# Performance work log

Measured on AMD Instinct MI355X. Metric: run time of the kernel, lower is better.

The kernel has to match this reference:

```python
import jax, jax.numpy as jnp
import numpy as np

E, H, F = 1024, 16, 4096
WH, WW = 32, 32
B = 4
L = WH * WW           # 1024 cross-attn kv tokens
N = L + 1             # 1025 decoder tokens (CLS + window)
D = E // H
SCALE = D ** -0.5
NEG = -1e9            # stands in for -inf in the causal mask


def _rel_coords(Wh, Ww):
    coords = np.stack(np.meshgrid(np.arange(Wh), np.arange(Ww), indexing='ij')).reshape(2, -1)
    rc = (coords[:, :, None] - coords[:, None, :]).transpose(1, 2, 0).astype(np.int64)
    rc[:, :, 0] += Wh - 1
    rc[:, :, 1] += Ww - 1
    rc[:, :, 0] *= 2 * Ww - 1
    return rc.sum(-1)  # (L, L)


def rel_index_self(Wh, Ww):
    nrd = (2 * Wh - 1) * (2 * Ww - 1) + 3
    l = Wh * Ww
    idx = np.zeros((l + 1, l + 1), dtype=np.int32)
    idx[1:, 1:] = _rel_coords(Wh, Ww)
    idx[0, :] = nrd - 3
    idx[:, 0] = nrd - 2
    idx[0, 0] = nrd - 1
    return idx


def rel_index_cross(Wh, Ww):
    nrd = (2 * Wh - 1) * (2 * Ww - 1) + 1
    l = Wh * Ww
    idx = np.zeros((l + 1, l), dtype=np.int32)
    idx[1:, :] = _rel_coords(Wh, Ww)
    idx[0, :] = nrd - 1
    return idx


IDX_SELF = jnp.asarray(rel_index_self(WH, WW))    # (N, N) int32
IDX_CROSS = jnp.asarray(rel_index_cross(WH, WW))  # (N, L) int32
CAUSAL = jnp.triu(jnp.full((N, N), NEG, jnp.float32), 1)


def _ln(x, g, b, eps=1e-5):
    m = x.mean(-1, keepdims=True)
    v = ((x - m) ** 2).mean(-1, keepdims=True)
    return (x - m) * jax.lax.rsqrt(v + eps) * g + b


def setup_inputs():
    key = jax.random.key(0)
    ks = jax.random.split(key, 24)
    g = lambda i, shape, s=0.02: jax.random.normal(ks[i], shape, jnp.float32) * s
    return dict(
        x=g(0, (B, N, E), 1.0),
        y=g(1, (B, L, E), 1.0),
        norm1_g=jnp.ones((E,), jnp.float32), norm1_b=jnp.zeros((E,), jnp.float32),
        norm2_g=jnp.ones((E,), jnp.float32), norm2_b=jnp.zeros((E,), jnp.float32),
        norm3_g=jnp.ones((E,), jnp.float32), norm3_b=jnp.zeros((E,), jnp.float32),
        sa_qkv_w=g(2, (3 * E, E)),
        sa_q_bias=g(3, (E,)),
        sa_v_bias=g(4, (E,)),
        sa_rpb=g(5, ((2 * WH - 1) * (2 * WW - 1) + 3, H)),
        sa_proj_w=g(6, (E, E)), sa_proj_b=g(7, (E,)),
        ca_q_w=g(8, (E, E)),
        ca_kv_w=g(9, (2 * E, E)),
        ca_q_bias=g(10, (E,)),
        ca_v_bias=g(11, (E,)),
        ca_rpb=g(12, ((2 * WH - 1) * (2 * WW - 1) + 1, H)),
        ca_proj_w=g(13, (E, E)), ca_proj_b=g(14, (E,)),
        fc1_w=g(15, (F, E)), fc1_b=g(16, (F,)),
        fc2_w=g(17, (E, F)), fc2_b=g(18, (E,)),
        gamma1=jnp.full((E,), 0.1, jnp.float32),
        gamma2=jnp.full((E,), 0.1, jnp.float32),
        gamma3=jnp.full((E,), 0.1, jnp.float32),
    )


def reference(x, y, norm1_g, norm1_b, norm2_g, norm2_b, norm3_g, norm3_b,
              sa_qkv_w, sa_q_bias, sa_v_bias, sa_rpb, sa_proj_w, sa_proj_b,
              ca_q_w, ca_kv_w, ca_q_bias, ca_v_bias, ca_rpb, ca_proj_w, ca_proj_b,
              fc1_w, fc1_b, fc2_w, fc2_b, gamma1, gamma2, gamma3):
    # cross_attn.extract_kv(y): k gets zero bias, v gets v_bias
    kv_bias = jnp.concatenate([jnp.zeros((E,), x.dtype), ca_v_bias])
    kv = (y @ ca_kv_w.T + kv_bias).reshape(B, L, 2, H, D)
    ck = kv[:, :, 0].transpose(0, 2, 1, 3)  # (B,H,L,D)
    cv = kv[:, :, 1].transpose(0, 2, 1, 3)

    # --- causal self-attention with gathered relative-position bias ---
    h = _ln(x, norm1_g, norm1_b)
    qkv_bias = jnp.concatenate([sa_q_bias, jnp.zeros((E,), x.dtype), sa_v_bias])
    qkv = (h @ sa_qkv_w.T + qkv_bias).reshape(B, N, 3, H, D)
    q = qkv[:, :, 0].transpose(0, 2, 1, 3) * SCALE  # (B,H,N,D)
    k = qkv[:, :, 1].transpose(0, 2, 1, 3)
    v = qkv[:, :, 2].transpose(0, 2, 1, 3)
    bias = sa_rpb[IDX_SELF].transpose(2, 0, 1) + CAUSAL  # (H,N,N)
    attn = jnp.einsum('bhqd,bhkd->bhqk', q, k) + bias[None]
    attn = jax.nn.softmax(attn, axis=-1)
    sa = jnp.einsum('bhqk,bhkd->bhqd', attn, v).transpose(0, 2, 1, 3).reshape(B, N, E)
    sa = sa @ sa_proj_w.T + sa_proj_b
    x = x + gamma1 * sa

    # --- cross-attention with gathered relative-position bias ---
    h = _ln(x, norm2_g, norm2_b)
    q = (h @ ca_q_w.T + ca_q_bias).reshape(B, N, H, D).transpose(0, 2, 1, 3) * SCALE
    cbias = ca_rpb[IDX_CROSS].transpose(2, 0, 1)  # (H,N,L)
    attn = jnp.einsum('bhqd,bhkd->bhqk', q, ck) + cbias[None]
    attn = jax.nn.softmax(attn, axis=-1)
    ca = jnp.einsum('bhqk,bhkd->bhqd', attn, cv).transpose(0, 2, 1, 3).reshape(B, N, E)
    ca = ca @ ca_proj_w.T + ca_proj_b
    x = x + gamma2 * ca

    # --- FFN (Linear -> GELU -> Linear, no inner identity) ---
    h = _ln(x, norm3_g, norm3_b)
    h = jax.nn.gelu(h @ fc1_w.T + fc1_b, approximate=False)
    h = h @ fc2_w.T + fc2_b
    x = x + gamma3 * h
    return x
```

## Files before the change

kernel.cpp:

```cpp
#include <hip/hip_runtime.h>
#include <hip/hip_bf16.h>
#include <math.h>

typedef __bf16 bf16;
typedef __bf16 bf16x8 __attribute__((ext_vector_type(8)));
typedef float f32x4 __attribute__((ext_vector_type(4)));

#define MP    4224
#define MACT  4100
#define NQTOK 1025
#define NKTOK 1024
#define EDIM  1024
#define FDIM  4096
#define NHEAD 16
#define HD    64
#define QSCALE 0.125f
#define VTS   1056

__device__ __forceinline__ void glds16(const bf16* g, bf16* l) {
  __builtin_amdgcn_global_load_lds(
      (const __attribute__((address_space(1))) void*)g,
      (__attribute__((address_space(3))) void*)l, 16, 0, 0);
}

__device__ __forceinline__ bf16x8 ld8(const void* p, size_t i, bool f32) {
  if (f32) {
    const float* q = (const float*)p + i;
    bf16x8 r;
#pragma unroll
    for (int j = 0; j < 8; ++j) r[j] = (bf16)q[j];
    return r;
  }
  return *(const bf16x8*)((const bf16*)p + i);
}

struct WPtrs { const float* s[8]; };
__global__ __launch_bounds__(256) void conv_kernel(WPtrs wp, bf16* dst) {
  const size_t sz[8] = {3145728UL, 1048576UL, 1048576UL, 2097152UL,
                        1048576UL, 4194304UL, 4194304UL, 4194304UL};
  size_t id = ((size_t)blockIdx.x * 256 + threadIdx.x) * 8;
  size_t off = 0;
#pragma unroll
  for (int i = 0; i < 8; ++i) {
    if (id < off + sz[i]) {
      const float* s = wp.s[i] + (id - off);
      bf16x8 r;
#pragma unroll
      for (int j = 0; j < 8; ++j) r[j] = (bf16)s[j];
      *(bf16x8*)(dst + id) = r;
      return;
    }
    off += sz[i];
  }
}

__global__ void zero_pads_kernel(bf16* hln) {
  int i = blockIdx.x * 256 + threadIdx.x;
  const int n = (MP - MACT) * EDIM;
  if (i < n) hln[(size_t)MACT * EDIM + i] = (bf16)0.0f;
}

template<bool FIRST>
__global__ __launch_bounds__(256) void ln_kernel(const float* __restrict__ src,
    float* __restrict__ xf, bf16* __restrict__ out,
    const float* __restrict__ g, const float* __restrict__ bta) {
  const int row = blockIdx.x;
  const int tid = threadIdx.x;
  float v[4];
#pragma unroll
  for (int i = 0; i < 4; ++i) {
    v[i] = src[(size_t)row * EDIM + tid + i * 256];
    if (FIRST) xf[(size_t)row * EDIM + tid + i * 256] = v[i];
  }
  float s = 0.f, sq = 0.f;
#pragma unroll
  for (int i = 0; i < 4; ++i) { s += v[i]; sq += v[i] * v[i]; }
#pragma unroll
  for (int m = 32; m >= 1; m >>= 1) {
    s += __shfl_xor(s, m);
    sq += __shfl_xor(sq, m);
  }
  __shared__ float ss[4], ssq[4];
  const int wave = tid >> 6;
  if ((tid & 63) == 0) { ss[wave] = s; ssq[wave] = sq; }
  __syncthreads();
  s = ss[0] + ss[1] + ss[2] + ss[3];
  sq = ssq[0] + ssq[1] + ssq[2] + ssq[3];
  const float mean = s * (1.f / EDIM);
  const float var = sq * (1.f / EDIM) - mean * mean;
  const float rstd = rsqrtf(var + 1e-5f);
#pragma unroll
  for (int i = 0; i < 4; ++i) {
    int e = tid + i * 256;
    out[(size_t)row * EDIM + e] = (bf16)((v[i] - mean) * rstd * g[e] + bta[e]);
  }
}

__global__ __launch_bounds__(256) void fc2_reduce_kernel(
    const float* __restrict__ p0, const float* __restrict__ xf,
    const float* __restrict__ bias, const float* __restrict__ gamma,
    float* __restrict__ outf) {
  size_t i = ((size_t)blockIdx.x * 256 + threadIdx.x) * 4;
  if (i >= (size_t)MACT * EDIM) return;
  f32x4 a = *(const f32x4*)(p0 + i);
  f32x4 b = *(const f32x4*)(outf + i);
  f32x4 x = *(const f32x4*)(xf + i);
  const int gn = (int)(i & (EDIM - 1));
  f32x4 r;
#pragma unroll
  for (int j = 0; j < 4; ++j)
    r[j] = x[j] + gamma[gn + j] * (a[j] + b[j] + bias[gn + j]);
  *(f32x4*)(outf + i) = r;
}

enum { EPI_QKV = 0, EPI_KV = 1, EPI_Q = 2, EPI_RES = 3, EPI_GELU = 4,
       EPI_FINAL = 5, EPI_PART = 6 };

template<int EPI, bool ASY>
__global__ __launch_bounds__(256) void gemm_bt(
    const void* __restrict__ A, const void* __restrict__ Bw,
    int K, int Kc,
    const float* __restrict__ bias0, const float* __restrict__ bias1,
    const float* __restrict__ gamma, float* __restrict__ xf,
    bf16* __restrict__ out0, bf16* __restrict__ out1, bf16* __restrict__ out2,
    float* __restrict__ outf)
{
  constexpr int LDP = ASY ? 32 : 40;
  __shared__ bf16 As[128][LDP];
  __shared__ bf16 Bs[128][LDP];
  const int tid = threadIdx.x;
  const int lane = tid & 63, wave = tid >> 6;
  const int quad = lane >> 4, l16 = lane & 15;
  const int wr = wave >> 1, wc = wave & 1;
  const int m0 = blockIdx.y * 128, n0 = blockIdx.x * 128;
  const int kbase = blockIdx.z * Kc;
  const bool first = (blockIdx.z == 0);
  const int r0 = tid >> 2, c0 = (tid & 3) * 8;

  const bf16* gA = nullptr; const bf16* gB = nullptr;
  bf16* lA = nullptr; bf16* lB = nullptr;
  if (ASY) {
    gA = (const bf16*)A + (size_t)(m0 + wave * 16 + (lane >> 2)) * K + kbase + (lane & 3) * 8;
    gB = (const bf16*)Bw + (size_t)(n0 + wave * 16 + (lane >> 2)) * K + kbase + (lane & 3) * 8;
    lA = &As[wave * 16][0];
    lB = &Bs[wave * 16][0];
  }

  f32x4 acc[4][4];
#pragma unroll
  for (int i = 0; i < 4; ++i)
#pragma unroll
    for (int j = 0; j < 4; ++j)
#pragma unroll
      for (int r = 0; r < 4; ++r) acc[i][j][r] = 0.f;

  for (int k0 = 0; k0 < Kc; k0 += 32) {
    if (ASY) {
      glds16(gA, lA);
      glds16(gA + (size_t)64 * K, lA + 64 * 32);
      glds16(gB, lB);
      glds16(gB + (size_t)64 * K, lB + 64 * 32);
      gA += 32; gB += 32;
    } else {
      const bool f32a = (EPI == EPI_KV);
      const size_t kk = (size_t)(kbase + k0);
      *(bf16x8*)(&As[r0][c0])      = ld8(A,  (size_t)(m0 + r0) * K + kk + c0, f32a);
      *(bf16x8*)(&As[r0 + 64][c0]) = ld8(A,  (size_t)(m0 + r0 + 64) * K + kk + c0, f32a);
      *(bf16x8*)(&Bs[r0][c0])      = ld8(Bw, (size_t)(n0 + r0) * K + kk + c0, true);
      *(bf16x8*)(&Bs[r0 + 64][c0]) = ld8(Bw, (size_t)(n0 + r0 + 64) * K + kk + c0, true);
    }
    __syncthreads();
    bf16x8 af[4], bfv[4];
#pragma unroll
    for (int i = 0; i < 4; ++i) {
      af[i]  = *(const bf16x8*)(&As[wr * 64 + i * 16 + l16][quad * 8]);
      bfv[i] = *(const bf16x8*)(&Bs[wc * 64 + i * 16 + l16][quad * 8]);
    }
#pragma unroll
    for (int mb = 0; mb < 4; ++mb)
#pragma unroll
      for (int nb = 0; nb < 4; ++nb)
        acc[mb][nb] = __builtin_amdgcn_mfma_f32_16x16x32_bf16(af[mb], bfv[nb], acc[mb][nb], 0, 0, 0);
    __syncthreads();
  }

#pragma unroll
  for (int mb = 0; mb < 4; ++mb) {
#pragma unroll
    for (int r = 0; r < 4; ++r) {
      const int gm = m0 + wr * 64 + mb * 16 + quad * 4 + r;
#pragma unroll
      for (int nb = 0; nb < 4; ++nb) {
        const int gn = n0 + wc * 64 + nb * 16 + l16;
        float v = acc[mb][nb][r];
        if (EPI == EPI_QKV) {
          if (gm < MACT) {
            unsigned b = (unsigned)gm / 1025u;
            unsigned t = (unsigned)gm - b * 1025u;
            int sec = gn >> 10, e = gn & 1023;
            int h = e >> 6, d = e & 63;
            if (sec == 0)
              out0[((size_t)(b * NHEAD + h) * NQTOK + t) * HD + d] =
                  (bf16)((v + bias0[e]) * QSCALE);
            else if (sec == 1)
              out1[((size_t)(b * NHEAD + h) * NQTOK + t) * HD + d] = (bf16)v;
            else
              out2[((size_t)(b * NHEAD + h) * HD + d) * VTS + t] =
                  (bf16)(v + bias1[e]);
          }
        } else if (EPI == EPI_KV) {
          unsigned b = (unsigned)gm >> 10;
          unsigned t = (unsigned)gm & 1023u;
          int sec = gn >> 10, e = gn & 1023;
          int h = e >> 6, d = e & 63;
          if (sec == 0)
            out0[((size_t)(b * NHEAD + h) * NKTOK + t) * HD + d] = (bf16)v;
          else
            out1[((size_t)(b * NHEAD + h) * HD + d) * NKTOK + t] =
                (bf16)(v + bias1[e]);
        } else if (EPI == EPI_Q) {
          if (gm < MACT) {
            unsigned b = (unsigned)gm / 1025u;
            unsigned t = (unsigned)gm - b * 1025u;
            int h = gn >> 6, d = gn & 63;
            outf[((size_t)(b * NHEAD + h) * NQTOK + t) * HD + d] =
                (v + bias0[gn]) * QSCALE;
          }
        } else if (EPI == EPI_RES) {
          if (gm < MACT) {
            size_t o = (size_t)gm * EDIM + gn;
            xf[o] += gamma[gn] * (v + bias0[gn]);
          }
        } else if (EPI == EPI_GELU) {
          float z = v + bias0[gn];
          float ge = 0.5f * z * (1.0f + erff(z * 0.70710678118f));
          out0[(size_t)gm * FDIM + gn] = (bf16)ge;
        } else if (EPI == EPI_PART) {
          if (gm < MACT) {
            float* dst = first ? xf : outf;
            dst[(size_t)gm * EDIM + gn] = v;
          }
        } else {
          if (gm < MACT) {
            size_t o = (size_t)gm * EDIM + gn;
            float add = gamma[gn] * (v + (first ? bias0[gn] : 0.f));
            if (first) add += xf[o];
            atomicAdd(&outf[o], add);
          }
        }
      }
    }
  }
}

template<bool CROSS>
__global__ __launch_bounds__(256) void attn_kernel(
    const void* __restrict__ Q, const bf16* __restrict__ Kg,
    const bf16* __restrict__ Vg, const float* __restrict__ rpb,
    bf16* __restrict__ out)
{
  const int NK  = CROSS ? NKTOK : NQTOK;
  const int NRD = CROSS ? 3970 : 3972;
  const int VS  = CROSS ? NKTOK : VTS;
  const int qt  = CROSS ? blockIdx.x : (16 - blockIdx.x);
  const int h = blockIdx.y, b = blockIdx.z;
  const int tid = threadIdx.x;
  const int lane = tid & 63, wave = tid >> 6;
  const int quad = lane >> 4, l16 = lane & 15;

  __shared__ bf16 rpb_s[4096];
  __shared__ bf16 Ks[64][72];
  __shared__ bf16 Vt[64][72];
  __shared__ bf16 Ps[4][16][72];

  for (int i = tid; i < 4096; i += 256)
    rpb_s[i] = (bf16)((i < NRD) ? rpb[(size_t)i * NHEAD + h] : 0.f);

  const int q0 = qt * 64;
  const int qrow = q0 + wave * 16 + l16;
  const size_t qhb = (size_t)(b * NHEAD + h) * NQTOK;
  bf16x8 qf0, qf1;
  if (qrow < NQTOK) {
    if (CROSS) {
      const float* Qf = (const float*)Q + (qhb + qrow) * HD;
#pragma unroll
      for (int j = 0; j < 8; ++j) {
        qf0[j] = (bf16)Qf[quad * 8 + j];
        qf1[j] = (bf16)Qf[32 + quad * 8 + j];
      }
    } else {
      const bf16* Qb = (const bf16*)Q;
      qf0 = *(const bf16x8*)(Qb + (qhb + qrow) * HD + quad * 8);
      qf1 = *(const bf16x8*)(Qb + (qhb + qrow) * HD + 32 + quad * 8);
    }
  } else {
#pragma unroll
    for (int j = 0; j < 8; ++j) { qf0[j] = (bf16)0.f; qf1[j] = (bf16)0.f; }
  }

  int qgv[4], qcode[4];
#pragma unroll
  for (int r = 0; r < 4; ++r) {
    int qg = q0 + wave * 16 + quad * 4 + r;
    qgv[r] = qg;
    int p = qg - 1;
    qcode[r] = (qg > 0) ? ((p >> 5) * 63 + (p & 31) + 1984) : 0;
  }

  float m_run[4], l_run[4];
  f32x4 oacc[4];
#pragma unroll
  for (int r = 0; r < 4; ++r) { m_run[r] = -1e30f; l_run[r] = 0.f; }
#pragma unroll
  for (int d = 0; d < 4; ++d)
#pragma unroll
    for (int r = 0; r < 4; ++r) oacc[d][r] = 0.f;

  const size_t kvbK = (size_t)(b * NHEAD + h) * NK;
  const size_t vbase = (size_t)(b * NHEAD + h) * HD;
  const int nch = CROSS ? (NKTOK / 64) : (qt + 1);

  const int rr = tid >> 3;
  const int co = (tid & 7) * 8;

  bf16x8 krg[2], vrg[2];
  auto stage_load = [&](int c) {
    const int kc = c * 64;
#pragma unroll
    for (int vv = 0; vv < 2; ++vv) {
      const int row = rr + vv * 32;
      if (!CROSS && kc + row >= NK) {
#pragma unroll
        for (int j = 0; j < 8; ++j) krg[vv][j] = (bf16)0.f;
      } else {
        krg[vv] = *(const bf16x8*)(Kg + (kvbK + kc + row) * HD + co);
      }
      if (!CROSS && kc + co >= NK) {
#pragma unroll
        for (int j = 0; j < 8; ++j) vrg[vv][j] = (bf16)0.f;
      } else {
        vrg[vv] = *(const bf16x8*)(Vg + (vbase + row) * VS + kc + co);
      }
    }
  };

  stage_load(0);
  for (int c = 0; c < nch; ++c) {
    const int kc = c * 64;
    if (c) __syncthreads();
#pragma unroll
    for (int vv = 0; vv < 2; ++vv) {
      const int row = rr + vv * 32;
      *(bf16x8*)(&Ks[row][co]) = krg[vv];
      *(bf16x8*)(&Vt[row][co]) = vrg[vv];
    }
    __syncthreads();
    if (c + 1 < nch) stage_load(c + 1);

    float sv[4][4];
#pragma unroll
    for (int kb = 0; kb < 4; ++kb) {
      f32x4 a;
#pragma unroll
      for (int r = 0; r < 4; ++r) a[r] = 0.f;
      bf16x8 kf0 = *(const bf16x8*)(&Ks[kb * 16 + l16][quad * 8]);
      bf16x8 kf1 = *(const bf16x8*)(&Ks[kb * 16 + l16][32 + quad * 8]);
      a = __builtin_amdgcn_mfma_f32_16x16x32_bf16(qf0, kf0, a, 0, 0, 0);
      a = __builtin_amdgcn_mfma_f32_16x16x32_bf16(qf1, kf1, a, 0, 0, 0);
      const int kg = kc + kb * 16 + l16;
      int kcode;
      if (CROSS) kcode = (kg >> 5) * 63 + (kg & 31);
      else {
        int k1 = kg - 1;
        kcode = (kg > 0) ? ((k1 >> 5) * 63 + (k1 & 31)) : 0;
      }
#pragma unroll
      for (int r = 0; r < 4; ++r) {
        const int qg = qgv[r];
        bool valid = (kg < NK) && (CROSS || kg <= qg);
        int idx;
        if (CROSS) {
          idx = (qg == 0) ? 3969 : (qcode[r] - kcode);
        } else {
          idx = (qg == 0) ? ((kg == 0) ? 3971 : 3969)
                          : ((kg == 0) ? 3970 : (qcode[r] - kcode));
        }
        sv[kb][r] = valid ? (a[r] + (float)rpb_s[idx]) : -1e30f;
      }
    }

#pragma unroll
    for (int r = 0; r < 4; ++r) {
      float mx = fmaxf(fmaxf(sv[0][r], sv[1][r]), fmaxf(sv[2][r], sv[3][r]));
#pragma unroll
      for (int mk = 8; mk >= 1; mk >>= 1) mx = fmaxf(mx, __shfl_xor(mx, mk));
      const float mnew = fmaxf(m_run[r], mx);
      const float alpha = __expf(m_run[r] - mnew);
      m_run[r] = mnew;
      float rs = 0.f;
#pragma unroll
      for (int kb = 0; kb < 4; ++kb) {
        float p = __expf(sv[kb][r] - mnew);
        rs += p;
        Ps[wave][quad * 4 + r][kb * 16 + l16] = (bf16)p;
      }
#pragma unroll
      for (int mk = 8; mk >= 1; mk >>= 1) rs += __shfl_xor(rs, mk);
      l_run[r] = l_run[r] * alpha + rs;
#pragma unroll
      for (int d = 0; d < 4; ++d) oacc[d][r] *= alpha;
    }

    bf16x8 pf0 = *(const bf16x8*)(&Ps[wave][l16][quad * 8]);
    bf16x8 pf1 = *(const bf16x8*)(&Ps[wave][l16][32 + quad * 8]);
#pragma unroll
    for (int db = 0; db < 4; ++db) {
      bf16x8 vf0 = *(const bf16x8*)(&Vt[db * 16 + l16][quad * 8]);
      bf16x8 vf1 = *(const bf16x8*)(&Vt[db * 16 + l16][32 + quad * 8]);
      oacc[db] = __builtin_amdgcn_mfma_f32_16x16x32_bf16(pf0, vf0, oacc[db], 0, 0, 0);
      oacc[db] = __builtin_amdgcn_mfma_f32_16x16x32_bf16(pf1, vf1, oacc[db], 0, 0, 0);
    }
  }

#pragma unroll
  for (int r = 0; r < 4; ++r) {
    const int qg = qgv[r];
    if (qg < NQTOK) {
      const float inv = 1.f / l_run[r];
      const size_t row = (size_t)b * NQTOK + qg;
#pragma unroll
      for (int db = 0; db < 4; ++db)
        out[row * EDIM + h * HD + db * 16 + l16] = (bf16)(oacc[db][r] * inv);
    }
  }
}

extern "C" void kernel_launch(void* const* d_in, const int* in_sizes, int n_in,
                              void* d_out, int out_size, void* d_ws, size_t ws_size,
                              hipStream_t stream) {
  (void)in_sizes; (void)n_in; (void)out_size;
  const float* x        = (const float*)d_in[0];
  const float* y        = (const float*)d_in[1];
  const float* n1g      = (const float*)d_in[2];
  const float* n1b      = (const float*)d_in[3];
  const float* n2g      = (const float*)d_in[4];
  const float* n2b      = (const float*)d_in[5];
  const float* n3g      = (const float*)d_in[6];
  const float* n3b      = (const float*)d_in[7];
  const float* sa_qkv_w = (const float*)d_in[8];
  const float* sa_qb    = (const float*)d_in[9];
  const float* sa_vb    = (const float*)d_in[10];
  const float* sa_rpb   = (const float*)d_in[11];
  const float* sa_pw    = (const float*)d_in[12];
  const float* sa_pb    = (const float*)d_in[13];
  const float* ca_qw    = (const float*)d_in[14];
  const float* ca_kvw   = (const float*)d_in[15];
  const float* ca_qb    = (const float*)d_in[16];
  const float* ca_vb    = (const float*)d_in[17];
  const float* ca_rpb   = (const float*)d_in[18];
  const float* ca_pw    = (const float*)d_in[19];
  const float* ca_pb    = (const float*)d_in[20];
  const float* fc1_w    = (const float*)d_in[21];
  const float* fc1_b    = (const float*)d_in[22];
  const float* fc2_w    = (const float*)d_in[23];
  const float* fc2_b    = (const float*)d_in[24];
  const float* g1       = (const float*)d_in[25];
  const float* g2       = (const float*)d_in[26];
  const float* g3       = (const float*)d_in[27];
  float* outf = (float*)d_out;
  float* qtf  = (float*)d_out;

  char* w = (char*)d_ws;
  float* xf = (float*)w;  w += (size_t)MP * EDIM * 4;
  bf16* hln = (bf16*)w;   w += (size_t)MP * EDIM * 2;
  char* big = w;          w += (size_t)MP * FDIM * 2;
  const size_t qkv_sz = (size_t)4 * NHEAD * NQTOK * HD * 2;
  bf16* qt = (bf16*)big;
  bf16* kt = (bf16*)(big + qkv_sz);
  bf16* vt = (bf16*)(big + 2 * qkv_sz);
  bf16* h1 = (bf16*)big;
  bf16* wpool = (bf16*)w; w += 20971520UL * 2;
  const bool asy = ((size_t)(w - (char*)d_ws) <= ws_size);

  bf16* qkvw_b = wpool;
  bf16* pw_b   = qkvw_b + 3145728UL;
  bf16* cqw_b  = pw_b   + 1048576UL;
  bf16* ckvw_b = cqw_b  + 1048576UL;
  bf16* cpw_b  = ckvw_b + 2097152UL;
  bf16* fc1w_b = cpw_b  + 1048576UL;
  bf16* fc2w_b = fc1w_b + 4194304UL;
  bf16* y_b    = fc2w_b + 4194304UL;
  float* part0 = (float*)wpool;

  if (asy) {
    WPtrs wp = {{sa_qkv_w, sa_pw, ca_qw, ca_kvw, ca_pw, fc1_w, fc2_w, y}};
    conv_kernel<<<10240, 256, 0, stream>>>(wp, wpool);
  }
  zero_pads_kernel<<<dim3(((MP - MACT) * EDIM + 255) / 256), 256, 0, stream>>>(hln);

  ln_kernel<true><<<MACT, 256, 0, stream>>>(x, xf, hln, n1g, n1b);
  if (asy) gemm_bt<EPI_QKV, true><<<dim3(24, 33, 1), 256, 0, stream>>>(hln, qkvw_b, 1024, 1024,
      sa_qb, sa_vb, nullptr, nullptr, qt, kt, vt, nullptr);
  else     gemm_bt<EPI_QKV, false><<<dim3(24, 33, 1), 256, 0, stream>>>(hln, sa_qkv_w, 1024, 1024,
      sa_qb, sa_vb, nullptr, nullptr, qt, kt, vt, nullptr);
  attn_kernel<false><<<dim3(17, NHEAD, 4), 256, 0, stream>>>(qt, kt, vt, sa_rpb, hln);
  if (asy) gemm_bt<EPI_RES, true><<<dim3(8, 33, 1), 256, 0, stream>>>(hln, pw_b, 1024, 1024,
      sa_pb, nullptr, g1, xf, nullptr, nullptr, nullptr, nullptr);
  else     gemm_bt<EPI_RES, false><<<dim3(8, 33, 1), 256, 0, stream>>>(hln, sa_pw, 1024, 1024,
      sa_pb, nullptr, g1, xf, nullptr, nullptr, nullptr, nullptr);

  ln_kernel<false><<<MACT, 256, 0, stream>>>(xf, nullptr, hln, n2g, n2b);
  if (asy) gemm_bt<EPI_Q, true><<<dim3(8, 33, 1), 256, 0, stream>>>(hln, cqw_b, 1024, 1024,
      ca_qb, nullptr, nullptr, nullptr, nullptr, nullptr, nullptr, qtf);
  else     gemm_bt<EPI_Q, false><<<dim3(8, 33, 1), 256, 0, stream>>>(hln, ca_qw, 1024, 1024,
      ca_qb, nullptr, nullptr, nullptr, nullptr, nullptr, nullptr, qtf);
  if (asy) gemm_bt<EPI_KV, true><<<dim3(16, 32, 1), 256, 0, stream>>>(y_b, ckvw_b, 1024, 1024,
      nullptr, ca_vb, nullptr, nullptr, kt, vt, nullptr, nullptr);
  else     gemm_bt<EPI_KV, false><<<dim3(16, 32, 1), 256, 0, stream>>>(y, ca_kvw, 1024, 1024,
      nullptr, ca_vb, nullptr, nullptr, kt, vt, nullptr, nullptr);
  attn_kernel<true><<<dim3(17, NHEAD, 4), 256, 0, stream>>>(qtf, kt, vt, ca_rpb, hln);
  if (asy) gemm_bt<EPI_RES, true><<<dim3(8, 33, 1), 256, 0, stream>>>(hln, cpw_b, 1024, 1024,
      ca_pb, nullptr, g2, xf, nullptr, nullptr, nullptr, nullptr);
  else     gemm_bt<EPI_RES, false><<<dim3(8, 33, 1), 256, 0, stream>>>(hln, ca_pw, 1024, 1024,
      ca_pb, nullptr, g2, xf, nullptr, nullptr, nullptr, nullptr);

  ln_kernel<false><<<MACT, 256, 0, stream>>>(xf, nullptr, hln, n3g, n3b);
  if (asy) gemm_bt<EPI_GELU, true><<<dim3(32, 33, 1), 256, 0, stream>>>(hln, fc1w_b, 1024, 1024,
      fc1_b, nullptr, nullptr, nullptr, h1, nullptr, nullptr, nullptr);
  else     gemm_bt<EPI_GELU, false><<<dim3(32, 33, 1), 256, 0, stream>>>(hln, fc1_w, 1024, 1024,
      fc1_b, nullptr, nullptr, nullptr, h1, nullptr, nullptr, nullptr);
  if (asy) {
    gemm_bt<EPI_PART, true><<<dim3(8, 33, 2), 256, 0, stream>>>(h1, fc2w_b, 4096, 2048,
        nullptr, nullptr, nullptr, part0, nullptr, nullptr, nullptr, outf);
    fc2_reduce_kernel<<<dim3(4100), 256, 0, stream>>>(part0, xf, fc2_b, g3, outf);
  } else {
    hipMemsetAsync(outf, 0, (size_t)MACT * EDIM * 4, stream);
    gemm_bt<EPI_FINAL, false><<<dim3(8, 33, 4), 256, 0, stream>>>(h1, fc2_w, 4096, 1024,
        fc2_b, nullptr, g3, xf, nullptr, nullptr, nullptr, outf);
  }
}
```

Baseline: 746.7 us.

## Transpose QK MFMA to keep P in registers and defer softmax rescaling

The QK^T MFMA now swaps its operands, so each lane holds scores for a single query row across several keys. That makes the row max and sum need only two cross-quad shuffles instead of per-row 16-lane reductions. The probabilities are packed to bf16 and redistributed with lane shuffles into the PV A-operand layout, which removes the Ps shared-memory round trip. The running-max rescale of the accumulator is skipped unless the new max exceeds the old by more than 8, trading some headroom in the exponent range for fewer rescales.

```diff
diff --git a/kernel.cpp b/kernel.cpp
--- a/kernel.cpp
+++ b/kernel.cpp
@@ -271,7 +271,6 @@
   __shared__ bf16 rpb_s[4096];
   __shared__ bf16 Ks[64][72];
   __shared__ bf16 Vt[64][72];
-  __shared__ bf16 Ps[4][16][72];
 
   for (int i = tid; i < 4096; i += 256)
     rpb_s[i] = (bf16)((i < NRD) ? rpb[(size_t)i * NHEAD + h] : 0.f);
@@ -298,19 +297,12 @@
     for (int j = 0; j < 8; ++j) { qf0[j] = (bf16)0.f; qf1[j] = (bf16)0.f; }
   }
 
-  int qgv[4], qcode[4];
-#pragma unroll
-  for (int r = 0; r < 4; ++r) {
-    int qg = q0 + wave * 16 + quad * 4 + r;
-    qgv[r] = qg;
-    int p = qg - 1;
-    qcode[r] = (qg > 0) ? ((p >> 5) * 63 + (p & 31) + 1984) : 0;
-  }
-
-  float m_run[4], l_run[4];
+  const int qg = qrow;
+  const int qp = qg - 1;
+  const int qcode = (qg > 0) ? ((qp >> 5) * 63 + (qp & 31) + 1984) : 0;
+
+  float m_run = -1e30f, l_run = 0.f;
   f32x4 oacc[4];
-#pragma unroll
-  for (int r = 0; r < 4; ++r) { m_run[r] = -1e30f; l_run[r] = 0.f; }
 #pragma unroll
   for (int d = 0; d < 4; ++d)
 #pragma unroll
@@ -322,6 +314,9 @@
 
   const int rr = tid >> 3;
   const int co = (tid & 7) * 8;
+
+  const int srcA = (quad & 1) * 32 + l16;
+  const int srcB = srcA + 16;
 
   bf16x8 krg[2], vrg[2];
   auto stage_load = [&](int c) {
@@ -365,69 +360,97 @@
       for (int r = 0; r < 4; ++r) a[r] = 0.f;
       bf16x8 kf0 = *(const bf16x8*)(&Ks[kb * 16 + l16][quad * 8]);
       bf16x8 kf1 = *(const bf16x8*)(&Ks[kb * 16 + l16][32 + quad * 8]);
-      a = __builtin_amdgcn_mfma_f32_16x16x32_bf16(qf0, kf0, a, 0, 0, 0);
-      a = __builtin_amdgcn_mfma_f32_16x16x32_bf16(qf1, kf1, a, 0, 0, 0);
-      const int kg = kc + kb * 16 + l16;
-      int kcode;
-      if (CROSS) kcode = (kg >> 5) * 63 + (kg & 31);
-      else {
-        int k1 = kg - 1;
-        kcode = (kg > 0) ? ((k1 >> 5) * 63 + (k1 & 31)) : 0;
-      }
+      a = __builtin_amdgcn_mfma_f32_16x16x32_bf16(kf0, qf0, a, 0, 0, 0);
+      a = __builtin_amdgcn_mfma_f32_16x16x32_bf16(kf1, qf1, a, 0, 0, 0);
 #pragma unroll
       for (int r = 0; r < 4; ++r) {
-        const int qg = qgv[r];
-        bool valid = (kg < NK) && (CROSS || kg <= qg);
+        const int kg = kc + kb * 16 + quad * 4 + r;
+        int kcode;
+        if (CROSS) kcode = (kg >> 5) * 63 + (kg & 31);
+        else {
+          int k1 = kg - 1;
+          kcode = (kg > 0) ? ((k1 >> 5) * 63 + (k1 & 31)) : 0;
+        }
+        bool valid = CROSS ? true : (kg < NK && kg <= qg);
         int idx;
         if (CROSS) {
-          idx = (qg == 0) ? 3969 : (qcode[r] - kcode);
+          idx = (qg == 0) ? 3969 : (qcode - kcode);
         } else {
           idx = (qg == 0) ? ((kg == 0) ? 3971 : 3969)
-                          : ((kg == 0) ? 3970 : (qcode[r] - kcode));
+                          : ((kg == 0) ? 3970 : (qcode - kcode));
         }
+        idx &= 4095;
         sv[kb][r] = valid ? (a[r] + (float)rpb_s[idx]) : -1e30f;
       }
     }
 
-#pragma unroll
-    for (int r = 0; r < 4; ++r) {
-      float mx = fmaxf(fmaxf(sv[0][r], sv[1][r]), fmaxf(sv[2][r], sv[3][r]));
-#pragma unroll
-      for (int mk = 8; mk >= 1; mk >>= 1) mx = fmaxf(mx, __shfl_xor(mx, mk));
-      const float mnew = fmaxf(m_run[r], mx);
-      const float alpha = __expf(m_run[r] - mnew);
-      m_run[r] = mnew;
-      float rs = 0.f;
-#pragma unroll
-      for (int kb = 0; kb < 4; ++kb) {
-        float p = __expf(sv[kb][r] - mnew);
-        rs += p;
-        Ps[wave][quad * 4 + r][kb * 16 + l16] = (bf16)p;
-      }
-#pragma unroll
-      for (int mk = 8; mk >= 1; mk >>= 1) rs += __shfl_xor(rs, mk);
-      l_run[r] = l_run[r] * alpha + rs;
-#pragma unroll
-      for (int d = 0; d < 4; ++d) oacc[d][r] *= alpha;
-    }
-
-    bf16x8 pf0 = *(const bf16x8*)(&Ps[wave][l16][quad * 8]);
-    bf16x8 pf1 = *(const bf16x8*)(&Ps[wave][l16][32 + quad * 8]);
+    float mx = sv[0][0];
+#pragma unroll
+    for (int kb = 0; kb < 4; ++kb)
+#pragma unroll
+      for (int r = 0; r < 4; ++r) mx = fmaxf(mx, sv[kb][r]);
+    mx = fmaxf(mx, __shfl_xor(mx, 16));
+    mx = fmaxf(mx, __shfl_xor(mx, 32));
+
+    if (!__all(mx - m_run <= 8.f)) {
+      const float mnew = fmaxf(m_run, mx);
+      const float alpha = __expf(m_run - mnew);
+      m_run = mnew;
+      l_run *= alpha;
+      float alr[4];
+#pragma unroll
+      for (int r = 0; r < 4; ++r) alr[r] = __shfl(alpha, quad * 4 + r);
+#pragma unroll
+      for (int d = 0; d < 4; ++d)
+#pragma unroll
+        for (int r = 0; r < 4; ++r) oacc[d][r] *= alr[r];
+    }
+
+    float rs = 0.f;
+    unsigned pk[4][2];
+#pragma unroll
+    for (int kb = 0; kb < 4; ++kb) {
+      float p0 = __expf(sv[kb][0] - m_run);
+      float p1 = __expf(sv[kb][1] - m_run);
+      float p2 = __expf(sv[kb][2] - m_run);
+      float p3 = __expf(sv[kb][3] - m_run);
+      rs += (p0 + p1) + (p2 + p3);
+      union { __bf16 h[2]; unsigned u; } w0, w1;
+      w0.h[0] = (bf16)p0; w0.h[1] = (bf16)p1;
+      w1.h[0] = (bf16)p2; w1.h[1] = (bf16)p3;
+      pk[kb][0] = w0.u; pk[kb][1] = w1.u;
+    }
+    rs += __shfl_xor(rs, 16);
+    rs += __shfl_xor(rs, 32);
+    l_run += rs;
+
+    union { unsigned u[4]; bf16x8 v; } f0, f1;
+#pragma unroll
+    for (int p = 0; p < 4; ++p) {
+      const int src = (p < 2) ? srcA : srcB;
+      unsigned a0 = (unsigned)__shfl((int)pk[0][p & 1], src);
+      unsigned a1 = (unsigned)__shfl((int)pk[1][p & 1], src);
+      unsigned b0 = (unsigned)__shfl((int)pk[2][p & 1], src);
+      unsigned b1 = (unsigned)__shfl((int)pk[3][p & 1], src);
+      f0.u[p] = (quad < 2) ? a0 : a1;
+      f1.u[p] = (quad < 2) ? b0 : b1;
+    }
+
 #pragma unroll
     for (int db = 0; db < 4; ++db) {
       bf16x8 vf0 = *(const bf16x8*)(&Vt[db * 16 + l16][quad * 8]);
       bf16x8 vf1 = *(const bf16x8*)(&Vt[db * 16 + l16][32 + quad * 8]);
-      oacc[db] = __builtin_amdgcn_mfma_f32_16x16x32_bf16(pf0, vf0, oacc[db], 0, 0, 0);
-      oacc[db] = __builtin_amdgcn_mfma_f32_16x16x32_bf16(pf1, vf1, oacc[db], 0, 0, 0);
+      oacc[db] = __builtin_amdgcn_mfma_f32_16x16x32_bf16(f0.v, vf0, oacc[db], 0, 0, 0);
+      oacc[db] = __builtin_amdgcn_mfma_f32_16x16x32_bf16(f1.v, vf1, oacc[db], 0, 0, 0);
     }
   }
 
 #pragma unroll
   for (int r = 0; r < 4; ++r) {
-    const int qg = qgv[r];
-    if (qg < NQTOK) {
-      const float inv = 1.f / l_run[r];
-      const size_t row = (size_t)b * NQTOK + qg;
+    const int qo = q0 + wave * 16 + quad * 4 + r;
+    if (qo < NQTOK) {
+      const float inv = 1.f / __shfl(l_run, quad * 4 + r);
+      const size_t row = (size_t)b * NQTOK + qo;
 #pragma unroll
       for (int db = 0; db < 4; ++db)
         out[row * EDIM + h * HD + db * 16 + l16] = (bf16)(oacc[db][r] * inv);
```

Result: faster. 719.7 us (-3.6%).
